# Performance work log

Measured on AMD Instinct MI355X. Metric: run time of the kernel, lower is better.

The kernel has to match this reference:

```python
import jax, jax.numpy as jnp
import numpy as np

NUM_EMBEDDINGS = 1024
EMBEDDING_DIM = 64
COMMITMENT_COST = 0.1
DECAY = 0.9
EPSILON = 1e-05


def setup_inputs() -> dict:
    key = jax.random.key(0)
    k1, k2, k3 = jax.random.split(key, 3)
    inputs = jax.random.normal(k1, (16, EMBEDDING_DIM, 4096), dtype=jnp.float32)
    embedding_weight = jax.random.normal(k2, (NUM_EMBEDDINGS, EMBEDDING_DIM), dtype=jnp.float32)
    ema_cluster_size = jnp.zeros((NUM_EMBEDDINGS,), dtype=jnp.float32)
    ema_w = jax.random.normal(k3, (NUM_EMBEDDINGS, EMBEDDING_DIM), dtype=jnp.float32)
    return {
        "inputs": inputs,
        "embedding_weight": embedding_weight,
        "ema_cluster_size": ema_cluster_size,
        "ema_w": ema_w,
    }


def reference(inputs, embedding_weight, ema_cluster_size, ema_w):
    K, D = embedding_weight.shape
    # (B, C, L) -> (B, L, C); C == embedding_dim
    x = jnp.transpose(inputs, (0, 2, 1))
    B, L, _ = x.shape
    flat = x.reshape(-1, D)  # [N, D], N = B*L
    N = flat.shape[0]

    distances = (
        jnp.sum(flat * flat, axis=1, keepdims=True)
        + jnp.sum(embedding_weight * embedding_weight, axis=1)
        - 2.0 * (flat @ embedding_weight.T)
    )
    idx = jnp.argmin(distances, axis=1)  # [N] int

    # embedding lookup (equivalent to one-hot @ weight)
    quantized = embedding_weight[idx].reshape(B, L, D)

    # one-hot column sums and scatter-reduction, without materializing [N, K]
    counts = jnp.zeros((K,), dtype=flat.dtype).at[idx].add(1.0)  # sum(encodings, 0)
    dw = jax.ops.segment_sum(flat, idx, num_segments=K)  # encodings^T @ flat_input

    # EMA updates (training path)
    cs = ema_cluster_size * DECAY + (1.0 - DECAY) * counts
    n = jnp.sum(cs)
    cs = (cs + EPSILON) / (n + K * EPSILON) * n
    new_ema_w = ema_w * DECAY + (1.0 - DECAY) * dw
    new_embedding_weight = new_ema_w / cs[:, None]

    # KLDivLoss(batchmean)(softmax(quantized.detach()), softmax(inputs)) over dim=2
    p_in = jax.nn.softmax(jax.lax.stop_gradient(quantized), axis=2)
    p_tgt = jax.nn.softmax(x, axis=2)
    kl = jnp.sum(p_tgt * (jnp.log(p_tgt) - p_in)) / B
    loss = COMMITMENT_COST * kl

    # straight-through estimator
    quantized_st = x + jax.lax.stop_gradient(quantized - x)

    avg_probs = counts / N
    perplexity = jnp.exp(-jnp.sum(avg_probs * jnp.log(avg_probs + 1e-10)))

    out = jnp.transpose(quantized_st, (0, 2, 1))  # back to (B, C, L)
    encoding_indices = idx[:, None]
    return (out, loss, perplexity, new_embedding_weight, encoding_indices)
```

## Files before the change

### kernel.cpp

```cpp
#include <hip/hip_runtime.h>

#define LDIM 4096
#define DDIM 64
#define KCODES 1024
#define BDIM 16
#define NROWS 65536
#define NSLICE 8
#define SLICE_ROWS (NROWS / NSLICE)

typedef __attribute__((ext_vector_type(8))) short short8;
typedef __attribute__((ext_vector_type(16))) float float16v;

__device__ __forceinline__ unsigned int orderf(float f) {
  unsigned int u = __float_as_uint(f);
  return (u & 0x80000000u) ? ~u : (u | 0x80000000u);
}

__device__ __forceinline__ unsigned long long shfl_xor_u64(unsigned long long v, int m) {
  int lo = __shfl_xor((int)(unsigned int)(v & 0xffffffffull), m, 64);
  int hi = __shfl_xor((int)(unsigned int)(v >> 32), m, 64);
  return ((unsigned long long)(unsigned int)hi << 32) | (unsigned int)lo;
}

__device__ __forceinline__ unsigned int bf16_rne(float x) {
  unsigned int u = __float_as_uint(x);
  return (u + 0x7FFFu + ((u >> 16) & 1u)) >> 16;
}

__global__ void prep_kernel(const float* __restrict__ Ew,
                            float* __restrict__ enorm,
                            float* __restrict__ SE,
                            unsigned short* __restrict__ Epk2) {
  int k = blockIdx.x;
  int d = threadIdx.x;
  float v = Ew[k * DDIM + d];
  float n2 = v * v;
  #pragma unroll
  for (int o = 32; o > 0; o >>= 1) n2 += __shfl_xor(n2, o, 64);
  float m = v;
  #pragma unroll
  for (int o = 32; o > 0; o >>= 1) m = fmaxf(m, __shfl_xor(m, o, 64));
  float e = __expf(v - m);
  float Z = e;
  #pragma unroll
  for (int o = 32; o > 0; o >>= 1) Z += __shfl_xor(Z, o, 64);
  SE[k * DDIM + d] = e / Z;
  if (d == 0) enorm[k] = n2;

  unsigned int rh = bf16_rne(v);
  float hif = __uint_as_float(rh << 16);
  unsigned int rl = bf16_rne(v - hif);
  int tile = k >> 5, mm = k & 31;
  int s = d >> 4, h = (d >> 3) & 1, j = d & 7;
  int base = tile * 4096 + (h * 32 + mm) * 8 + j;
  Epk2[base + s * 512]        = (unsigned short)rh;
  Epk2[base + (4 + s) * 512]  = (unsigned short)rl;
}

__launch_bounds__(256, 2)
__global__ void argmin_fused_kernel(const float* __restrict__ inp,
                                    const unsigned short* __restrict__ Epk2,
                                    const float* __restrict__ enorm,
                                    const float* __restrict__ SE,
                                    const float* __restrict__ Ew,
                                    int* __restrict__ idx_ws,
                                    float* __restrict__ outidx,
                                    float* __restrict__ out,
                                    float* __restrict__ klacc) {
  const int tid = threadIdx.x;
  const int lane = tid & 63;
  const int w = tid >> 6;
  const int half = lane >> 5;
  const int m = lane & 31;
  const int row_base = blockIdx.x * 128 + w * 32;
  const int b = row_base >> 12;
  const int l0 = row_base & 4095;
  const float* xp = inp + (size_t)b * DDIM * LDIM + l0 + m;

  short8 afr[8];
  float ex[4][8];
  float Zp = 0.f, S1p = 0.f;
  #pragma unroll
  for (int s = 0; s < 4; s++) {
    #pragma unroll
    for (int j = 0; j < 8; j++) {
      int d = 16 * s + 8 * half + j;
      float x = xp[(size_t)d * LDIM];
      float e = __expf(x);
      ex[s][j] = e;
      Zp += e;
      S1p = fmaf(e, x, S1p);
      unsigned int rh = bf16_rne(x);
      float hif = __uint_as_float(rh << 16);
      unsigned int rl = bf16_rne(x - hif);
      afr[s][j] = (short)(unsigned short)rh;
      afr[4 + s][j] = (short)(unsigned short)rl;
    }
  }

  float bsc[16];
  int bix[16];
  #pragma unroll
  for (int j = 0; j < 16; j++) { bsc[j] = 1e30f; bix[j] = 0; }

  const unsigned short* eb = Epk2 + lane * 8;

  short8 bA[8], bB[8];
  float enA, enB;

  float16v zacc = {};

  #pragma unroll
  for (int s = 0; s < 4; s++) {
    bA[s]     = *(const short8*)(eb + s * 512);
    bA[4 + s] = *(const short8*)(eb + 2048 + s * 512);
  }
  enA = enorm[m];

  #pragma unroll 1
  for (int i = 0; i < 16; i++) {
    const int tB = 2 * i + 1;
    {
      const unsigned short* p = eb + tB * 4096;
      #pragma unroll
      for (int s = 0; s < 4; s++) {
        bB[s]     = *(const short8*)(p + s * 512);
        bB[4 + s] = *(const short8*)(p + 2048 + s * 512);
      }
      enB = enorm[tB * 32 + m];
    }
    {
      float16v acc = __builtin_amdgcn_mfma_f32_32x32x16_bf16(afr[0], bA[0], zacc, 0, 0, 0);
      acc = __builtin_amdgcn_mfma_f32_32x32x16_bf16(afr[0], bA[4], acc, 0, 0, 0);
      acc = __builtin_amdgcn_mfma_f32_32x32x16_bf16(afr[4], bA[0], acc, 0, 0, 0);
      #pragma unroll
      for (int s = 1; s < 4; s++) {
        acc = __builtin_amdgcn_mfma_f32_32x32x16_bf16(afr[s], bA[s], acc, 0, 0, 0);
        acc = __builtin_amdgcn_mfma_f32_32x32x16_bf16(afr[s], bA[4 + s], acc, 0, 0, 0);
        acc = __builtin_amdgcn_mfma_f32_32x32x16_bf16(afr[4 + s], bA[s], acc, 0, 0, 0);
      }
      int ci = 2 * i * 32 + m;
      #pragma unroll
      for (int j = 0; j < 16; j++) {
        float sc = fmaf(-2.f, acc[j], enA);
        if (sc < bsc[j]) { bsc[j] = sc; bix[j] = ci; }
      }
    }
    if (i < 15) {
      const unsigned short* p = eb + (2 * i + 2) * 4096;
      #pragma unroll
      for (int s = 0; s < 4; s++) {
        bA[s]     = *(const short8*)(p + s * 512);
        bA[4 + s] = *(const short8*)(p + 2048 + s * 512);
      }
      enA = enorm[(2 * i + 2) * 32 + m];
    }
    {
      float16v acc = __builtin_amdgcn_mfma_f32_32x32x16_bf16(afr[0], bB[0], zacc, 0, 0, 0);
      acc = __builtin_amdgcn_mfma_f32_32x32x16_bf16(afr[0], bB[4], acc, 0, 0, 0);
      acc = __builtin_amdgcn_mfma_f32_32x32x16_bf16(afr[4], bB[0], acc, 0, 0, 0);
      #pragma unroll
      for (int s = 1; s < 4; s++) {
        acc = __builtin_amdgcn_mfma_f32_32x32x16_bf16(afr[s], bB[s], acc, 0, 0, 0);
        acc = __builtin_amdgcn_mfma_f32_32x32x16_bf16(afr[s], bB[4 + s], acc, 0, 0, 0);
        acc = __builtin_amdgcn_mfma_f32_32x32x16_bf16(afr[4 + s], bB[s], acc, 0, 0, 0);
      }
      int ci = tB * 32 + m;
      #pragma unroll
      for (int j = 0; j < 16; j++) {
        float sc = fmaf(-2.f, acc[j], enB);
        if (sc < bsc[j]) { bsc[j] = sc; bix[j] = ci; }
      }
    }
  }

  const int jr = (m & 3) | ((m >> 3) << 2);
  const int hr = (m >> 2) & 1;
  unsigned long long mykey = 0ull;

  #pragma unroll
  for (int j = 0; j < 16; j++) {
    unsigned long long key =
        ((unsigned long long)orderf(bsc[j]) << 32) | (unsigned int)bix[j];
    #pragma unroll
    for (int mm = 1; mm < 32; mm <<= 1) {
      unsigned long long o = shfl_xor_u64(key, mm);
      if (o < key) key = o;
    }
    if (j == jr) mykey = key;
  }
  unsigned long long partner = shfl_xor_u64(mykey, 32);
  unsigned long long keyrow = (hr == half) ? mykey : partner;
  const int kr = (int)(keyrow & 0xffffffffull);

  if (half == 0) {
    idx_ws[row_base + m] = kr;
    outidx[row_base + m] = (float)kr;
  }

  float Up = 0.f;
  const float* sebase = SE + kr * DDIM + 8 * half;
  const float* ewbase = Ew + kr * DDIM + 8 * half;
  float* obase = out + (size_t)b * DDIM * LDIM + l0 + m;
  #pragma unroll
  for (int s = 0; s < 4; s++) {
    float4 q0 = *(const float4*)(sebase + 16 * s);
    float4 q1 = *(const float4*)(sebase + 16 * s + 4);
    Up = fmaf(ex[s][0], q0.x, Up); Up = fmaf(ex[s][1], q0.y, Up);
    Up = fmaf(ex[s][2], q0.z, Up); Up = fmaf(ex[s][3], q0.w, Up);
    Up = fmaf(ex[s][4], q1.x, Up); Up = fmaf(ex[s][5], q1.y, Up);
    Up = fmaf(ex[s][6], q1.z, Up); Up = fmaf(ex[s][7], q1.w, Up);
    float4 e0 = *(const float4*)(ewbase + 16 * s);
    float4 e1 = *(const float4*)(ewbase + 16 * s + 4);
    const int d0 = 16 * s + 8 * half;
    obase[(size_t)(d0 + 0) * LDIM] = e0.x;
    obase[(size_t)(d0 + 1) * LDIM] = e0.y;
    obase[(size_t)(d0 + 2) * LDIM] = e0.z;
    obase[(size_t)(d0 + 3) * LDIM] = e0.w;
    obase[(size_t)(d0 + 4) * LDIM] = e1.x;
    obase[(size_t)(d0 + 5) * LDIM] = e1.y;
    obase[(size_t)(d0 + 6) * LDIM] = e1.z;
    obase[(size_t)(d0 + 7) * LDIM] = e1.w;
  }

  float Z = Zp + __shfl_xor(Zp, 32, 64);
  float S1 = S1p + __shfl_xor(S1p, 32, 64);
  float U = Up + __shfl_xor(Up, 32, 64);
  float kl = (S1 - U) / Z - __logf(Z);
  kl = (half == 0) ? kl : 0.f;
  #pragma unroll
  for (int o = 1; o < 64; o <<= 1) kl += __shfl_xor(kl, o, 64);
  if (lane == 0) atomicAdd(klacc, kl);
}

__launch_bounds__(256)
__global__ void dw_kernel(const float* __restrict__ inp,
                          const int* __restrict__ idx_ws,
                          float* __restrict__ partial,
                          float* __restrict__ pcounts) {
  __shared__ float dwp[KCODES];
  __shared__ float cnt[KCODES];
  const int tid = threadIdx.x;
  const int d = blockIdx.x & 63;
  const int slice = blockIdx.x >> 6;
  const bool do_cnt = (d == 0);

  #pragma unroll
  for (int i = 0; i < KCODES / 256; i++) {
    dwp[tid + i * 256] = 0.f;
    cnt[tid + i * 256] = 0.f;
  }
  __syncthreads();

  const int r0 = slice * SLICE_ROWS;
  #pragma unroll 1
  for (int j = 0; j < 8; j++) {
    const int rbase = r0 + j * 1024 + tid * 4;
    const int bb = rbase >> 12;
    const int ll = rbase & 4095;
    const float4 xv = *(const float4*)(inp + (size_t)bb * DDIM * LDIM +
                                       (size_t)d * LDIM + ll);
    const int4 kv = *(const int4*)(idx_ws + rbase);
    atomicAdd(&dwp[kv.x], xv.x);
    atomicAdd(&dwp[kv.y], xv.y);
    atomicAdd(&dwp[kv.z], xv.z);
    atomicAdd(&dwp[kv.w], xv.w);
    if (do_cnt) {
      atomicAdd(&cnt[kv.x], 1.0f);
      atomicAdd(&cnt[kv.y], 1.0f);
      atomicAdd(&cnt[kv.z], 1.0f);
      atomicAdd(&cnt[kv.w], 1.0f);
    }
  }
  __syncthreads();

  float* dst = partial + ((size_t)slice * 64 + d) * KCODES;
  #pragma unroll
  for (int i = 0; i < KCODES / 256; i++) dst[tid + i * 256] = dwp[tid + i * 256];
  if (do_cnt) {
    float* cd = pcounts + (size_t)slice * KCODES;
    #pragma unroll
    for (int i = 0; i < KCODES / 256; i++) cd[tid + i * 256] = cnt[tid + i * 256];
  }
}

__launch_bounds__(256)
__global__ void finalize_kernel(const float* __restrict__ partial,
                                const float* __restrict__ pcounts,
                                const float* __restrict__ emaw,
                                const float* __restrict__ emacs,
                                const float* __restrict__ klacc,
                                float* __restrict__ emb_out,
                                float* __restrict__ loss_out,
                                float* __restrict__ perp_out) {
  __shared__ float red[4], red2[4];
  const int tid = threadIdx.x;
  const int i = blockIdx.x * 256 + tid;
  const int k = i >> 6, d = i & 63;

  float se = 0.f;
  #pragma unroll
  for (int t = 0; t < 4; t++) se += emacs[tid * 4 + t];
  #pragma unroll
  for (int o = 32; o > 0; o >>= 1) se += __shfl_xor(se, o, 64);
  if ((tid & 63) == 0) red[tid >> 6] = se;
  __syncthreads();
  const float S = red[0] + red[1] + red[2] + red[3];
  const float N = 0.9f * S + 0.1f * (float)NROWS;

  float c = 0.f;
  #pragma unroll
  for (int sl = 0; sl < NSLICE; sl++) c += pcounts[sl * KCODES + k];
  float cs = fmaf(0.1f, c, emacs[k] * 0.9f);
  float csp = (cs + 1e-5f) / (N + (float)KCODES * 1e-5f) * N;

  float s = 0.f;
  #pragma unroll
  for (int sl = 0; sl < NSLICE; sl++)
    s += partial[((size_t)sl * 64 + d) * KCODES + k];
  emb_out[i] = fmaf(0.1f, s, emaw[i] * 0.9f) / csp;

  if (blockIdx.x == 0) {
    float es = 0.f;
    #pragma unroll
    for (int t = 0; t < 4; t++) {
      int kk = tid * 4 + t;
      float cc = 0.f;
      #pragma unroll
      for (int sl = 0; sl < NSLICE; sl++) cc += pcounts[sl * KCODES + kk];
      float a = cc * (1.0f / (float)NROWS);
      es += a * logf(a + 1e-10f);
    }
    #pragma unroll
    for (int o = 32; o > 0; o >>= 1) es += __shfl_xor(es, o, 64);
    if ((tid & 63) == 0) red2[tid >> 6] = es;
    __syncthreads();
    if (tid == 0) {
      *perp_out = expf(-(red2[0] + red2[1] + red2[2] + red2[3]));
      *loss_out = 0.1f * (*klacc) * (1.0f / 16.0f);
    }
  }
}

extern "C" void kernel_launch(void* const* d_in, const int* in_sizes, int n_in,
                              void* d_out, int out_size, void* d_ws, size_t ws_size,
                              hipStream_t stream) {
  const float* inp   = (const float*)d_in[0];
  const float* Ew    = (const float*)d_in[1];
  const float* emacs = (const float*)d_in[2];
  const float* emaw  = (const float*)d_in[3];

  float* out      = (float*)d_out;
  float* loss_out = out + 4194304;
  float* perp_out = out + 4194305;
  float* emb_out  = out + 4194306;
  float* idxf_out = out + 4194306 + 65536;

  char* ws = (char*)d_ws;
  int*   idx_ws  = (int*)(ws);
  float* klacc   = (float*)(ws + 262144);
  float* enorm   = (float*)(ws + 266496);
  float* SE      = (float*)(ws + 274688);
  unsigned short* Epk2 = (unsigned short*)(ws + 536832);
  float* partial = (float*)(ws + 536832);
  float* pcounts = (float*)(ws + 2633984);

  hipMemsetAsync(ws + 262144, 0, 256, stream);

  prep_kernel<<<KCODES, 64, 0, stream>>>(Ew, enorm, SE, Epk2);
  argmin_fused_kernel<<<512, 256, 0, stream>>>(inp, Epk2, enorm, SE, Ew,
                                               idx_ws, idxf_out, out, klacc);
  dw_kernel<<<512, 256, 0, stream>>>(inp, idx_ws, partial, pcounts);
  finalize_kernel<<<NROWS / 256, 256, 0, stream>>>(partial, pcounts, emaw, emacs,
                                                   klacc, emb_out, loss_out,
                                                   perp_out);
}
```

Before: 176.0 us.

## Split codebook search across wave pairs and widen dw kernel blocks

The argmin kernel now assigns each 32-row group to two waves, each scanning half of the codebook. The two partial minima are merged through shared memory. The launch doubles to 1024 blocks, with launch bounds raised to 4 blocks per SU. After the merge, one wave computes the KL term and the other writes the quantized output, splitting the epilogue work. The dw kernel moves to 512-thread blocks with a fully unrolled 4-iteration loop. The aim is more parallelism and latency hiding in the MFMA search. The cost is that each wave loads and converts the input rows redundantly, plus two block barriers and a tighter register budget.

```diff
diff --git a/kernel.cpp b/kernel.cpp
--- a/kernel.cpp
+++ b/kernel.cpp
@@ -57,7 +57,7 @@
   Epk2[base + (4 + s) * 512]  = (unsigned short)rl;
 }
 
-__launch_bounds__(256, 2)
+__launch_bounds__(256, 4)
 __global__ void argmin_fused_kernel(const float* __restrict__ inp,
                                     const unsigned short* __restrict__ Epk2,
                                     const float* __restrict__ enorm,
@@ -67,12 +67,17 @@
                                     float* __restrict__ outidx,
                                     float* __restrict__ out,
                                     float* __restrict__ klacc) {
+  __shared__ unsigned long long lkeys[2][32];
+  __shared__ int fkr[2][32];
+
   const int tid = threadIdx.x;
   const int lane = tid & 63;
   const int w = tid >> 6;
+  const int wp = w >> 1;
+  const int kh = w & 1;
   const int half = lane >> 5;
   const int m = lane & 31;
-  const int row_base = blockIdx.x * 128 + w * 32;
+  const int row_base = blockIdx.x * 64 + wp * 32;
   const int b = row_base >> 12;
   const int l0 = row_base & 4095;
   const float* xp = inp + (size_t)b * DDIM * LDIM + l0 + m;
@@ -103,11 +108,11 @@
   #pragma unroll
   for (int j = 0; j < 16; j++) { bsc[j] = 1e30f; bix[j] = 0; }
 
-  const unsigned short* eb = Epk2 + lane * 8;
+  const unsigned short* eb = Epk2 + (size_t)(kh * 16) * 4096 + lane * 8;
+  const int kbase = kh * 512;
 
   short8 bA[8], bB[8];
   float enA, enB;
-
   float16v zacc = {};
 
   #pragma unroll
@@ -115,19 +120,19 @@
     bA[s]     = *(const short8*)(eb + s * 512);
     bA[4 + s] = *(const short8*)(eb + 2048 + s * 512);
   }
-  enA = enorm[m];
+  enA = enorm[kbase + m];
 
   #pragma unroll 1
-  for (int i = 0; i < 16; i++) {
+  for (int i = 0; i < 8; i++) {
     const int tB = 2 * i + 1;
     {
-      const unsigned short* p = eb + tB * 4096;
+      const unsigned short* p = eb + (size_t)tB * 4096;
       #pragma unroll
       for (int s = 0; s < 4; s++) {
         bB[s]     = *(const short8*)(p + s * 512);
         bB[4 + s] = *(const short8*)(p + 2048 + s * 512);
       }
-      enB = enorm[tB * 32 + m];
+      enB = enorm[kbase + tB * 32 + m];
     }
     {
       float16v acc = __builtin_amdgcn_mfma_f32_32x32x16_bf16(afr[0], bA[0], zacc, 0, 0, 0);
@@ -139,21 +144,21 @@
         acc = __builtin_amdgcn_mfma_f32_32x32x16_bf16(afr[s], bA[4 + s], acc, 0, 0, 0);
         acc = __builtin_amdgcn_mfma_f32_32x32x16_bf16(afr[4 + s], bA[s], acc, 0, 0, 0);
       }
-      int ci = 2 * i * 32 + m;
+      int ci = kbase + 2 * i * 32 + m;
       #pragma unroll
       for (int j = 0; j < 16; j++) {
         float sc = fmaf(-2.f, acc[j], enA);
         if (sc < bsc[j]) { bsc[j] = sc; bix[j] = ci; }
       }
     }
-    if (i < 15) {
-      const unsigned short* p = eb + (2 * i + 2) * 4096;
+    if (i < 7) {
+      const unsigned short* p = eb + (size_t)(2 * i + 2) * 4096;
       #pragma unroll
       for (int s = 0; s < 4; s++) {
         bA[s]     = *(const short8*)(p + s * 512);
         bA[4 + s] = *(const short8*)(p + 2048 + s * 512);
       }
-      enA = enorm[(2 * i + 2) * 32 + m];
+      enA = enorm[kbase + (2 * i + 2) * 32 + m];
     }
     {
       float16v acc = __builtin_amdgcn_mfma_f32_32x32x16_bf16(afr[0], bB[0], zacc, 0, 0, 0);
@@ -165,7 +170,7 @@
         acc = __builtin_amdgcn_mfma_f32_32x32x16_bf16(afr[s], bB[4 + s], acc, 0, 0, 0);
         acc = __builtin_amdgcn_mfma_f32_32x32x16_bf16(afr[4 + s], bB[s], acc, 0, 0, 0);
       }
-      int ci = tB * 32 + m;
+      int ci = kbase + tB * 32 + m;
       #pragma unroll
       for (int j = 0; j < 16; j++) {
         float sc = fmaf(-2.f, acc[j], enB);
@@ -191,49 +196,66 @@
   }
   unsigned long long partner = shfl_xor_u64(mykey, 32);
   unsigned long long keyrow = (hr == half) ? mykey : partner;
-  const int kr = (int)(keyrow & 0xffffffffull);
-
-  if (half == 0) {
-    idx_ws[row_base + m] = kr;
-    outidx[row_base + m] = (float)kr;
-  }
-
-  float Up = 0.f;
-  const float* sebase = SE + kr * DDIM + 8 * half;
-  const float* ewbase = Ew + kr * DDIM + 8 * half;
-  float* obase = out + (size_t)b * DDIM * LDIM + l0 + m;
-  #pragma unroll
-  for (int s = 0; s < 4; s++) {
-    float4 q0 = *(const float4*)(sebase + 16 * s);
-    float4 q1 = *(const float4*)(sebase + 16 * s + 4);
-    Up = fmaf(ex[s][0], q0.x, Up); Up = fmaf(ex[s][1], q0.y, Up);
-    Up = fmaf(ex[s][2], q0.z, Up); Up = fmaf(ex[s][3], q0.w, Up);
-    Up = fmaf(ex[s][4], q1.x, Up); Up = fmaf(ex[s][5], q1.y, Up);
-    Up = fmaf(ex[s][6], q1.z, Up); Up = fmaf(ex[s][7], q1.w, Up);
-    float4 e0 = *(const float4*)(ewbase + 16 * s);
-    float4 e1 = *(const float4*)(ewbase + 16 * s + 4);
-    const int d0 = 16 * s + 8 * half;
-    obase[(size_t)(d0 + 0) * LDIM] = e0.x;
-    obase[(size_t)(d0 + 1) * LDIM] = e0.y;
-    obase[(size_t)(d0 + 2) * LDIM] = e0.z;
-    obase[(size_t)(d0 + 3) * LDIM] = e0.w;
-    obase[(size_t)(d0 + 4) * LDIM] = e1.x;
-    obase[(size_t)(d0 + 5) * LDIM] = e1.y;
-    obase[(size_t)(d0 + 6) * LDIM] = e1.z;
-    obase[(size_t)(d0 + 7) * LDIM] = e1.w;
-  }
-
-  float Z = Zp + __shfl_xor(Zp, 32, 64);
-  float S1 = S1p + __shfl_xor(S1p, 32, 64);
-  float U = Up + __shfl_xor(Up, 32, 64);
-  float kl = (S1 - U) / Z - __logf(Z);
-  kl = (half == 0) ? kl : 0.f;
-  #pragma unroll
-  for (int o = 1; o < 64; o <<= 1) kl += __shfl_xor(kl, o, 64);
-  if (lane == 0) atomicAdd(klacc, kl);
-}
-
-__launch_bounds__(256)
+
+  if (kh == 1) {
+    if (half == 0) lkeys[wp][m] = keyrow;
+  }
+  __syncthreads();
+  int kr = 0;
+  if (kh == 0) {
+    unsigned long long other = lkeys[wp][m];
+    if (other < keyrow) keyrow = other;
+    kr = (int)(keyrow & 0xffffffffull);
+    if (half == 0) {
+      idx_ws[row_base + m] = kr;
+      outidx[row_base + m] = (float)kr;
+      fkr[wp][m] = kr;
+    }
+  }
+  __syncthreads();
+
+  if (kh == 0) {
+    float Up = 0.f;
+    const float* sebase = SE + kr * DDIM + 8 * half;
+    #pragma unroll
+    for (int s = 0; s < 4; s++) {
+      float4 q0 = *(const float4*)(sebase + 16 * s);
+      float4 q1 = *(const float4*)(sebase + 16 * s + 4);
+      Up = fmaf(ex[s][0], q0.x, Up); Up = fmaf(ex[s][1], q0.y, Up);
+      Up = fmaf(ex[s][2], q0.z, Up); Up = fmaf(ex[s][3], q0.w, Up);
+      Up = fmaf(ex[s][4], q1.x, Up); Up = fmaf(ex[s][5], q1.y, Up);
+      Up = fmaf(ex[s][6], q1.z, Up); Up = fmaf(ex[s][7], q1.w, Up);
+    }
+    float Z = Zp + __shfl_xor(Zp, 32, 64);
+    float S1 = S1p + __shfl_xor(S1p, 32, 64);
+    float U = Up + __shfl_xor(Up, 32, 64);
+    float kl = (S1 - U) / Z - __logf(Z);
+    kl = (half == 0) ? kl : 0.f;
+    #pragma unroll
+    for (int o = 1; o < 64; o <<= 1) kl += __shfl_xor(kl, o, 64);
+    if (lane == 0) atomicAdd(klacc, kl);
+  } else {
+    int kro = fkr[wp][m];
+    const float* ewbase = Ew + kro * DDIM + 8 * half;
+    float* obase = out + (size_t)b * DDIM * LDIM + l0 + m;
+    #pragma unroll
+    for (int s = 0; s < 4; s++) {
+      float4 e0 = *(const float4*)(ewbase + 16 * s);
+      float4 e1 = *(const float4*)(ewbase + 16 * s + 4);
+      const int d0 = 16 * s + 8 * half;
+      obase[(size_t)(d0 + 0) * LDIM] = e0.x;
+      obase[(size_t)(d0 + 1) * LDIM] = e0.y;
+      obase[(size_t)(d0 + 2) * LDIM] = e0.z;
+      obase[(size_t)(d0 + 3) * LDIM] = e0.w;
+      obase[(size_t)(d0 + 4) * LDIM] = e1.x;
+      obase[(size_t)(d0 + 5) * LDIM] = e1.y;
+      obase[(size_t)(d0 + 6) * LDIM] = e1.z;
+      obase[(size_t)(d0 + 7) * LDIM] = e1.w;
+    }
+  }
+}
+
+__launch_bounds__(512)
 __global__ void dw_kernel(const float* __restrict__ inp,
                           const int* __restrict__ idx_ws,
                           float* __restrict__ partial,
@@ -246,16 +268,16 @@
   const bool do_cnt = (d == 0);
 
   #pragma unroll
-  for (int i = 0; i < KCODES / 256; i++) {
-    dwp[tid + i * 256] = 0.f;
-    cnt[tid + i * 256] = 0.f;
+  for (int i = 0; i < KCODES / 512; i++) {
+    dwp[tid + i * 512] = 0.f;
+    cnt[tid + i * 512] = 0.f;
   }
   __syncthreads();
 
   const int r0 = slice * SLICE_ROWS;
-  #pragma unroll 1
-  for (int j = 0; j < 8; j++) {
-    const int rbase = r0 + j * 1024 + tid * 4;
+  #pragma unroll
+  for (int j = 0; j < 4; j++) {
+    const int rbase = r0 + j * 2048 + tid * 4;
     const int bb = rbase >> 12;
     const int ll = rbase & 4095;
     const float4 xv = *(const float4*)(inp + (size_t)bb * DDIM * LDIM +
@@ -276,11 +298,11 @@
 
   float* dst = partial + ((size_t)slice * 64 + d) * KCODES;
   #pragma unroll
-  for (int i = 0; i < KCODES / 256; i++) dst[tid + i * 256] = dwp[tid + i * 256];
+  for (int i = 0; i < KCODES / 512; i++) dst[tid + i * 512] = dwp[tid + i * 512];
   if (do_cnt) {
     float* cd = pcounts + (size_t)slice * KCODES;
     #pragma unroll
-    for (int i = 0; i < KCODES / 256; i++) cd[tid + i * 256] = cnt[tid + i * 256];
+    for (int i = 0; i < KCODES / 512; i++) cd[tid + i * 512] = cnt[tid + i * 512];
   }
 }
 
@@ -368,9 +390,9 @@
   hipMemsetAsync(ws + 262144, 0, 256, stream);
 
   prep_kernel<<<KCODES, 64, 0, stream>>>(Ew, enorm, SE, Epk2);
-  argmin_fused_kernel<<<512, 256, 0, stream>>>(inp, Epk2, enorm, SE, Ew,
-                                               idx_ws, idxf_out, out, klacc);
-  dw_kernel<<<512, 256, 0, stream>>>(inp, idx_ws, partial, pcounts);
+  argmin_fused_kernel<<<1024, 256, 0, stream>>>(inp, Epk2, enorm, SE, Ew,
+                                                idx_ws, idxf_out, out, klacc);
+  dw_kernel<<<512, 512, 0, stream>>>(inp, idx_ws, partial, pcounts);
   finalize_kernel<<<NROWS / 256, 256, 0, stream>>>(partial, pcounts, emaw, emacs,
                                                    klacc, emb_out, loss_out,
                                                    perp_out);
```

Result: slower. 240.6 us (+36.7%).

## Stage codebook chunks in LDS, split MFMA chains, widen dw blocks

Applied to the files above, without the earlier changes.

The argmin kernel now copies 256-code chunks of the packed bf16 codebook (64 KB) into shared memory, where all four waves read them, instead of each wave loading its own copy from global memory. Each tile's three bf16 hi/lo product terms now go into three independent accumulators, which shortens the dependent MFMA chain. The dw kernel moves to 512 threads per block with a fully unrolled row loop. The 64 KB of LDS and the extra barriers can cut occupancy and remove the overlap the old software-prefetch double buffering gave.

```diff
diff --git a/kernel.cpp b/kernel.cpp
--- a/kernel.cpp
+++ b/kernel.cpp
@@ -67,6 +67,8 @@
                                     float* __restrict__ outidx,
                                     float* __restrict__ out,
                                     float* __restrict__ klacc) {
+  __shared__ unsigned short cbuf[32768];
+
   const int tid = threadIdx.x;
   const int lane = tid & 63;
   const int w = tid >> 6;
@@ -103,75 +105,48 @@
   #pragma unroll
   for (int j = 0; j < 16; j++) { bsc[j] = 1e30f; bix[j] = 0; }
 
-  const unsigned short* eb = Epk2 + lane * 8;
-
-  short8 bA[8], bB[8];
-  float enA, enB;
-
   float16v zacc = {};
 
-  #pragma unroll
-  for (int s = 0; s < 4; s++) {
-    bA[s]     = *(const short8*)(eb + s * 512);
-    bA[4 + s] = *(const short8*)(eb + 2048 + s * 512);
-  }
-  enA = enorm[m];
-
   #pragma unroll 1
-  for (int i = 0; i < 16; i++) {
-    const int tB = 2 * i + 1;
+  for (int q = 0; q < 4; q++) {
     {
-      const unsigned short* p = eb + tB * 4096;
+      const short8* src = (const short8*)Epk2 + (size_t)q * 4096;
+      short8* dst = (short8*)cbuf;
+      #pragma unroll
+      for (int it = 0; it < 16; it++) {
+        dst[it * 256 + tid] = src[it * 256 + tid];
+      }
+    }
+    __syncthreads();
+
+    #pragma unroll 1
+    for (int t = 0; t < 8; t++) {
+      const unsigned short* cb = cbuf + t * 4096 + lane * 8;
+      short8 bA[8];
       #pragma unroll
       for (int s = 0; s < 4; s++) {
-        bB[s]     = *(const short8*)(p + s * 512);
-        bB[4 + s] = *(const short8*)(p + 2048 + s * 512);
+        bA[s]     = *(const short8*)(cb + s * 512);
+        bA[4 + s] = *(const short8*)(cb + 2048 + s * 512);
       }
-      enB = enorm[tB * 32 + m];
-    }
-    {
-      float16v acc = __builtin_amdgcn_mfma_f32_32x32x16_bf16(afr[0], bA[0], zacc, 0, 0, 0);
-      acc = __builtin_amdgcn_mfma_f32_32x32x16_bf16(afr[0], bA[4], acc, 0, 0, 0);
-      acc = __builtin_amdgcn_mfma_f32_32x32x16_bf16(afr[4], bA[0], acc, 0, 0, 0);
+      float en = enorm[q * 256 + t * 32 + m];
+
+      float16v a0 = __builtin_amdgcn_mfma_f32_32x32x16_bf16(afr[0], bA[0], zacc, 0, 0, 0);
+      float16v a1 = __builtin_amdgcn_mfma_f32_32x32x16_bf16(afr[0], bA[4], zacc, 0, 0, 0);
+      float16v a2 = __builtin_amdgcn_mfma_f32_32x32x16_bf16(afr[4], bA[0], zacc, 0, 0, 0);
       #pragma unroll
       for (int s = 1; s < 4; s++) {
-        acc = __builtin_amdgcn_mfma_f32_32x32x16_bf16(afr[s], bA[s], acc, 0, 0, 0);
-        acc = __builtin_amdgcn_mfma_f32_32x32x16_bf16(afr[s], bA[4 + s], acc, 0, 0, 0);
-        acc = __builtin_amdgcn_mfma_f32_32x32x16_bf16(afr[4 + s], bA[s], acc, 0, 0, 0);
+        a0 = __builtin_amdgcn_mfma_f32_32x32x16_bf16(afr[s], bA[s], a0, 0, 0, 0);
+        a1 = __builtin_amdgcn_mfma_f32_32x32x16_bf16(afr[s], bA[4 + s], a1, 0, 0, 0);
+        a2 = __builtin_amdgcn_mfma_f32_32x32x16_bf16(afr[4 + s], bA[s], a2, 0, 0, 0);
       }
-      int ci = 2 * i * 32 + m;
+      int ci = q * 256 + t * 32 + m;
       #pragma unroll
       for (int j = 0; j < 16; j++) {
-        float sc = fmaf(-2.f, acc[j], enA);
+        float sc = fmaf(-2.f, a0[j] + a1[j] + a2[j], en);
         if (sc < bsc[j]) { bsc[j] = sc; bix[j] = ci; }
       }
     }
-    if (i < 15) {
-      const unsigned short* p = eb + (2 * i + 2) * 4096;
-      #pragma unroll
-      for (int s = 0; s < 4; s++) {
-        bA[s]     = *(const short8*)(p + s * 512);
-        bA[4 + s] = *(const short8*)(p + 2048 + s * 512);
-      }
-      enA = enorm[(2 * i + 2) * 32 + m];
-    }
-    {
-      float16v acc = __builtin_amdgcn_mfma_f32_32x32x16_bf16(afr[0], bB[0], zacc, 0, 0, 0);
-      acc = __builtin_amdgcn_mfma_f32_32x32x16_bf16(afr[0], bB[4], acc, 0, 0, 0);
-      acc = __builtin_amdgcn_mfma_f32_32x32x16_bf16(afr[4], bB[0], acc, 0, 0, 0);
-      #pragma unroll
-      for (int s = 1; s < 4; s++) {
-        acc = __builtin_amdgcn_mfma_f32_32x32x16_bf16(afr[s], bB[s], acc, 0, 0, 0);
-        acc = __builtin_amdgcn_mfma_f32_32x32x16_bf16(afr[s], bB[4 + s], acc, 0, 0, 0);
-        acc = __builtin_amdgcn_mfma_f32_32x32x16_bf16(afr[4 + s], bB[s], acc, 0, 0, 0);
-      }
-      int ci = tB * 32 + m;
-      #pragma unroll
-      for (int j = 0; j < 16; j++) {
-        float sc = fmaf(-2.f, acc[j], enB);
-        if (sc < bsc[j]) { bsc[j] = sc; bix[j] = ci; }
-      }
-    }
+    __syncthreads();
   }
 
   const int jr = (m & 3) | ((m >> 3) << 2);
@@ -233,7 +208,7 @@
   if (lane == 0) atomicAdd(klacc, kl);
 }
 
-__launch_bounds__(256)
+__launch_bounds__(512)
 __global__ void dw_kernel(const float* __restrict__ inp,
                           const int* __restrict__ idx_ws,
                           float* __restrict__ partial,
@@ -246,16 +221,16 @@
   const bool do_cnt = (d == 0);
 
   #pragma unroll
-  for (int i = 0; i < KCODES / 256; i++) {
-    dwp[tid + i * 256] = 0.f;
-    cnt[tid + i * 256] = 0.f;
+  for (int i = 0; i < KCODES / 512; i++) {
+    dwp[tid + i * 512] = 0.f;
+    cnt[tid + i * 512] = 0.f;
   }
   __syncthreads();
 
   const int r0 = slice * SLICE_ROWS;
-  #pragma unroll 1
-  for (int j = 0; j < 8; j++) {
-    const int rbase = r0 + j * 1024 + tid * 4;
+  #pragma unroll
+  for (int j = 0; j < 4; j++) {
+    const int rbase = r0 + j * 2048 + tid * 4;
     const int bb = rbase >> 12;
     const int ll = rbase & 4095;
     const float4 xv = *(const float4*)(inp + (size_t)bb * DDIM * LDIM +
@@ -276,11 +251,11 @@
 
   float* dst = partial + ((size_t)slice * 64 + d) * KCODES;
   #pragma unroll
-  for (int i = 0; i < KCODES / 256; i++) dst[tid + i * 256] = dwp[tid + i * 256];
+  for (int i = 0; i < KCODES / 512; i++) dst[tid + i * 512] = dwp[tid + i * 512];
   if (do_cnt) {
     float* cd = pcounts + (size_t)slice * KCODES;
     #pragma unroll
-    for (int i = 0; i < KCODES / 256; i++) cd[tid + i * 256] = cnt[tid + i * 256];
+    for (int i = 0; i < KCODES / 512; i++) cd[tid + i * 512] = cnt[tid + i * 512];
   }
 }
 
@@ -370,7 +345,7 @@
   prep_kernel<<<KCODES, 64, 0, stream>>>(Ew, enorm, SE, Epk2);
   argmin_fused_kernel<<<512, 256, 0, stream>>>(inp, Epk2, enorm, SE, Ew,
                                                idx_ws, idxf_out, out, klacc);
-  dw_kernel<<<512, 256, 0, stream>>>(inp, idx_ws, partial, pcounts);
+  dw_kernel<<<512, 512, 0, stream>>>(inp, idx_ws, partial, pcounts);
   finalize_kernel<<<NROWS / 256, 256, 0, stream>>>(partial, pcounts, emaw, emacs,
                                                    klacc, emb_out, loss_out,
                                                    perp_out);
```

Result: slower. 180.6 us (+2.6%).
